# Performance work log

Hardware: AMD Instinct MI355X
Metric: run time of the kernel (lower is better)

The kernel has to match this reference:

```python
import jax, jax.numpy as jnp
import numpy as np

B, T, D = 8, 2048, 1024
H, C, DV = 8, 64, 128   # n_heads, latent_dim, d_head
LN_EPS = 1e-5
NORM_EPS = 1e-12  # F.normalize eps


def _xavier(k, shape, fan_in, fan_out):
    lim = float(np.sqrt(6.0 / (fan_in + fan_out)))
    return jax.random.uniform(k, shape, jnp.float32, -lim, lim)


def setup_inputs() -> dict:
    key = jax.random.key(0)
    ks = jax.random.split(key, 9)
    x = jax.random.normal(ks[0], (B, T, D), jnp.float32)
    Wq = _xavier(ks[1], (C, D), D, C)            # S_q weight (out,in)
    Wk = _xavier(ks[2], (C, D), D, C)            # S_k
    Wv = _xavier(ks[3], (C, D), D, C)            # S_v
    Qc = _xavier(ks[4], (H, C, C), C, C)         # per-head latent rotations
    Vc = _xavier(ks[5], (H, C, DV), C, DV)       # per-head value up-proj
    Wa_w = _xavier(ks[6], (H * C, D), D, H * C)  # W_alpha weight
    Wa_b = jnp.full((H * C,), 3.0, jnp.float32)  # W_alpha bias init = 3.0
    Wo = _xavier(ks[7], (D, H * DV), H * DV, D)  # output proj
    gamma = jnp.ones((D,), jnp.float32)
    beta = jnp.zeros((D,), jnp.float32)
    return {"x": x, "Wq": Wq, "Wk": Wk, "Wv": Wv, "Qc": Qc, "Vc": Vc,
            "Wa_w": Wa_w, "Wa_b": Wa_b, "Wo": Wo, "gamma": gamma, "beta": beta}


def _forward(x, Wq, Wk, Wv, Qc, Vc, Wa_w, Wa_b, Wo, gamma, beta):
    residual = x
    # LayerNorm (biased variance, like torch)
    mu = jnp.mean(x, axis=-1, keepdims=True)
    var = jnp.mean(jnp.square(x - mu), axis=-1, keepdims=True)
    xn = (x - mu) * jax.lax.rsqrt(var + LN_EPS) * gamma + beta

    q_lat = xn @ Wq.T          # (B,T,C)
    k_lat = xn @ Wk.T          # (B,T,C) shared across heads
    v_lat = xn @ Wv.T          # (B,T,C)

    q = jnp.einsum('btc,hce->bhte', q_lat, Qc)   # (B,H,T,C)
    v = jnp.einsum('btc,hcd->bhtd', v_lat, Vc)   # (B,H,T,DV)
    alpha = jax.nn.sigmoid(xn @ Wa_w.T + Wa_b)   # (B,T,H*C)
    alpha = alpha.reshape(x.shape[0], x.shape[1], H, C).transpose(0, 2, 1, 3)  # (B,H,T,C)

    # F.normalize(k, dim=-1): k / max(||k||, eps)
    kn = k_lat / jnp.maximum(jnp.linalg.norm(k_lat, axis=-1, keepdims=True), NORM_EPS)

    # time-major for scan
    qs = jnp.moveaxis(q, 2, 0)      # (T,B,H,C)
    vs = jnp.moveaxis(v, 2, 0)      # (T,B,H,DV)
    als = jnp.moveaxis(alpha, 2, 0)  # (T,B,H,C)
    kns = jnp.moveaxis(kn, 1, 0)    # (T,B,C)

    S0 = jnp.zeros((x.shape[0], H, C, DV), x.dtype)

    def step(S, inp):
        q_t, k_t, v_t, a_t = inp
        # S_t = diag(alpha_t) S_{t-1} + k_t v_t^T  (k shared across heads)
        S = a_t[..., None] * S + k_t[:, None, :, None] * v_t[..., None, :]
        o_t = jnp.einsum('bhcv,bhc->bhv', S, q_t)
        return S, o_t

    _, outs = jax.lax.scan(step, S0, (qs, kns, vs, als))  # outs: (T,B,H,DV)
    out = jnp.moveaxis(outs, 0, 1).reshape(x.shape[0], x.shape[1], H * DV)
    return out @ Wo.T + residual


def reference(x, Wq, Wk, Wv, Qc, Vc, Wa_w, Wa_b, Wo, gamma, beta):
    return _forward(x, Wq, Wk, Wv, Qc, Vc, Wa_w, Wa_b, Wo, gamma, beta)
```

## Files before the change

kernel.cpp:

```cpp
#include <hip/hip_runtime.h>

typedef unsigned short u16;
typedef unsigned int   u32;
typedef __bf16 bf16x8 __attribute__((ext_vector_type(8)));
typedef float  f32x4  __attribute__((ext_vector_type(4)));
typedef float  f32x8  __attribute__((ext_vector_type(8)));

#define B_  8
#define T_  2048
#define D_  1024
#define H_  8
#define C_  64
#define DV_ 128
#define M_  (B_*T_)
#define L_  128
#define NC_ (T_/L_)

__device__ __forceinline__ u16 f2bf(float f){
  u32 u = __float_as_uint(f);
  u32 r = (u + 0x7fffu + ((u >> 16) & 1u)) >> 16;
  return (u16)r;
}
__device__ __forceinline__ float bf2f(u16 u){
  return __uint_as_float(((u32)u) << 16);
}

typedef const __attribute__((address_space(1))) unsigned int* gp1_t;
typedef __attribute__((address_space(3))) unsigned int* lp3_t;
__device__ __forceinline__ void stage16(const void* g, void* l){
  __builtin_amdgcn_global_load_lds((gp1_t)g, (lp3_t)l, 16, 0, 0);
}

__global__ __launch_bounds__(256) void ln_kernel(
    const float* __restrict__ x, const float* __restrict__ gamma,
    const float* __restrict__ beta, u16* __restrict__ xnb){
  const int m = blockIdx.x;
  const int tid = threadIdx.x;
  const int wave = tid >> 6, lane = tid & 63;
  const float* xr = x + (size_t)m * D_;
  float4 xv = *(const float4*)&xr[tid*4];
  float s = xv.x + xv.y + xv.z + xv.w;
  #pragma unroll
  for (int off = 32; off > 0; off >>= 1) s += __shfl_xor(s, off, 64);
  __shared__ float red[8];
  if (lane == 0) red[wave] = s;
  __syncthreads();
  float mu = (red[0]+red[1]+red[2]+red[3]) * (1.f/1024.f);
  float dx = xv.x-mu, dy = xv.y-mu, dz = xv.z-mu, dw = xv.w-mu;
  float ss = dx*dx + dy*dy + dz*dz + dw*dw;
  #pragma unroll
  for (int off = 32; off > 0; off >>= 1) ss += __shfl_xor(ss, off, 64);
  if (lane == 0) red[4+wave] = ss;
  __syncthreads();
  float var = (red[4]+red[5]+red[6]+red[7]) * (1.f/1024.f);
  float rs = rsqrtf(var + 1e-5f);
  float4 g  = *(const float4*)&gamma[tid*4];
  float4 bb = *(const float4*)&beta[tid*4];
  ushort4 o4;
  o4.x = f2bf(dx*rs*g.x + bb.x);
  o4.y = f2bf(dy*rs*g.y + bb.y);
  o4.z = f2bf(dz*rs*g.z + bb.z);
  o4.w = f2bf(dw*rs*g.w + bb.w);
  *(ushort4*)&xnb[(size_t)m*D_ + tid*4] = o4;
}

__global__ __launch_bounds__(256) void prep_weights(
    const float* __restrict__ Wq, const float* __restrict__ Wk,
    const float* __restrict__ Wv, const float* __restrict__ Wa,
    const float* __restrict__ Qc, const float* __restrict__ Vc,
    const float* __restrict__ Wo,
    u16* __restrict__ Wcatb, u16* __restrict__ QcTb,
    u16* __restrict__ VcTb,  u16* __restrict__ Wob){
  int idx = blockIdx.x * 256 + threadIdx.x;
  if (idx < 786432){
    int r = idx >> 10, col = idx & 1023;
    float v = 0.f;
    if (r < 64)       v = Wq[(size_t)r*1024 + col];
    else if (r < 128) v = Wk[(size_t)(r-64)*1024 + col];
    else if (r < 192) v = Wv[(size_t)(r-128)*1024 + col];
    else if (r < 704) v = Wa[(size_t)(r-192)*1024 + col];
    Wcatb[idx] = f2bf(v);
  } else if (idx < 819200){
    int i = idx - 786432;
    int n = i >> 6, c = i & 63; int h = n >> 6, e = n & 63;
    QcTb[i] = f2bf(Qc[((size_t)h*64 + c)*64 + e]);
  } else if (idx < 884736){
    int i = idx - 819200;
    int n = i >> 6, c = i & 63; int h = n >> 7, d = n & 127;
    VcTb[i] = f2bf(Vc[((size_t)h*64 + c)*128 + d]);
  } else {
    int i = idx - 884736;
    Wob[i] = f2bf(Wo[i]);
  }
}

__global__ __launch_bounds__(256) void gemm_bf16(
    const u16* __restrict__ A, const u16* __restrict__ Bw,
    float* __restrict__ C, const float* __restrict__ res,
    u16* __restrict__ Cb, int N, int K){
  __shared__ __align__(16) u16 As[2][128*32];
  __shared__ __align__(16) u16 Bs[2][128*32];
  const int tid = threadIdx.x;
  const int wave = tid >> 6;
  const int lane = tid & 63;
  const int q  = lane >> 4;
  const int mr = lane & 15;
  const int wr = wave >> 1, wc = wave & 1;

  const int gx = gridDim.x;
  const int nlin = blockIdx.y * gx + blockIdx.x;
  const int chunk = (gx * gridDim.y) >> 3;
  const int swz = (nlin & 7) * chunk + (nlin >> 3);
  const int m0 = (swz % gx) * 128;
  const int n0 = (swz / gx) * 128;

  const int j0 = wave*2;
  const int lr = lane >> 2;
  const int slg = ((lane & 3) ^ ((lr >> 1) & 3)) * 8;
  const u16* pa0 = A  + (size_t)(m0 + (j0  )*16 + lr)*K + slg;
  const u16* pa1 = A  + (size_t)(m0 + (j0+1)*16 + lr)*K + slg;
  const u16* pb0 = Bw + (size_t)(n0 + (j0  )*16 + lr)*K + slg;
  const u16* pb1 = Bw + (size_t)(n0 + (j0+1)*16 + lr)*K + slg;
  u16* la0 = &As[0][(j0  )*512];
  u16* la1 = &As[0][(j0+1)*512];
  u16* lb0 = &Bs[0][(j0  )*512];
  u16* lb1 = &Bs[0][(j0+1)*512];
  const int bufstride = 128*32;

  union FragU { uint4 u4; bf16x8 v; };
  f32x4 zero = {0.f, 0.f, 0.f, 0.f};
  f32x4 acc[4][4];
  #pragma unroll
  for (int i = 0; i < 4; i++)
    #pragma unroll
    for (int j = 0; j < 4; j++) acc[i][j] = zero;

  const int qs = (q ^ ((mr >> 1) & 3)) * 8;
  const int aoff = (wr*64 + mr)*32 + qs;
  const int boff = (wc*64 + mr)*32 + qs;

  stage16(pa0, la0); stage16(pa1, la1);
  stage16(pb0, lb0); stage16(pb1, lb1);
  __syncthreads();

  int p = 0;
  for (int k0 = 0; k0 < K; k0 += 32){
    if (k0 + 32 < K){
      int pn = p ^ 1;
      stage16(pa0 + k0 + 32, la0 + pn*bufstride);
      stage16(pa1 + k0 + 32, la1 + pn*bufstride);
      stage16(pb0 + k0 + 32, lb0 + pn*bufstride);
      stage16(pb1 + k0 + 32, lb1 + pn*bufstride);
    }
    bf16x8 afr[4], bfr[4];
    #pragma unroll
    for (int mt = 0; mt < 4; mt++){
      FragU f; f.u4 = *(const uint4*)(&As[p][aoff + mt*512]);
      afr[mt] = f.v;
    }
    #pragma unroll
    for (int nt = 0; nt < 4; nt++){
      FragU f; f.u4 = *(const uint4*)(&Bs[p][boff + nt*512]);
      bfr[nt] = f.v;
    }
    #pragma unroll
    for (int mt = 0; mt < 4; mt++)
      #pragma unroll
      for (int nt = 0; nt < 4; nt++)
        acc[mt][nt] = __builtin_amdgcn_mfma_f32_16x16x32_bf16(
            afr[mt], bfr[nt], acc[mt][nt], 0, 0, 0);
    __syncthreads();
    p ^= 1;
  }

  #pragma unroll
  for (int mt = 0; mt < 4; mt++)
    #pragma unroll
    for (int nt = 0; nt < 4; nt++){
      int col = n0 + wc*64 + nt*16 + mr;
      if (col < N){
        #pragma unroll
        for (int r = 0; r < 4; r++){
          int row = m0 + wr*64 + mt*16 + q*4 + r;
          size_t idx = (size_t)row * N + col;
          float v = acc[mt][nt][r];
          if (res) v += res[idx];
          if (Cb) Cb[idx] = f2bf(v);
          else    C[idx] = v;
        }
      }
    }
}

__global__ __launch_bounds__(256) void split_proj(
    const float* __restrict__ proj, const float* __restrict__ Wab,
    u16* __restrict__ qlatb, float* __restrict__ knf,
    u16* __restrict__ vlatb, float* __restrict__ alphaf){
  const int m = blockIdx.x * 4 + (threadIdx.x >> 6);
  const int lane = threadIdx.x & 63;
  const float* pr = proj + (size_t)m * 704;
  qlatb[(size_t)m*64 + lane] = f2bf(pr[lane]);
  float kv = pr[64 + lane];
  float ss = kv * kv;
  #pragma unroll
  for (int off = 32; off > 0; off >>= 1) ss += __shfl_xor(ss, off, 64);
  float nrm = fmaxf(sqrtf(ss), 1e-12f);
  knf[(size_t)m*64 + lane] = kv / nrm;
  vlatb[(size_t)m*64 + lane] = f2bf(pr[128 + lane]);
  #pragma unroll
  for (int j = 0; j < 8; j++){
    int jj = j*64 + lane;
    float av = pr[192 + jj] + Wab[jj];
    alphaf[(size_t)m*512 + jj] = 1.f / (1.f + expf(-av));
  }
}


__global__ __launch_bounds__(512, 8) void scan_pass1(
    const float* __restrict__ knf, const u16* __restrict__ vb,
    const float* __restrict__ alphaf,
    float* __restrict__ Sbuf, float* __restrict__ btot){
  const int ch = blockIdx.x;
  const int bh = blockIdx.y;
  const int b = bh >> 3, h = bh & 7;
  const int tid = threadIdx.x;
  const int w = __builtin_amdgcn_readfirstlane(tid >> 6);
  const int dg = tid & 63;
  const int t0 = ch * L_;

  const float* kp  = knf    + ((size_t)(b*T_ + t0))*64  + w*8;
  const float* ap  = alphaf + ((size_t)(b*T_ + t0))*512 + h*64 + w*8;
  const float* alp = ap + (dg & 7);
  const u32*   vp  = (const u32*)(vb + ((size_t)(b*T_ + t0))*1024 + h*128) + dg;

  float S[8][2];
  #pragma unroll
  for (int j = 0; j < 8; j++){ S[j][0] = 0.f; S[j][1] = 0.f; }
  float bt = 1.f;

  for (int t = 0; t < L_; t += 2){
    f32x8 a0, a1, k0, k1;
    asm volatile(
      "s_load_dwordx8 %0, %4, 0x0\n\t"
      "s_load_dwordx8 %1, %4, 0x800\n\t"
      "s_load_dwordx8 %2, %5, 0x0\n\t"
      "s_load_dwordx8 %3, %5, 0x100\n\t"
      "s_waitcnt lgkmcnt(0)"
      : "=&s"(a0), "=&s"(a1), "=&s"(k0), "=&s"(k1)
      : "s"(ap), "s"(kp));
    float al0 = alp[0], al1 = alp[512];
    u32 vv0 = vp[0], vv1 = vp[512];
    float v00 = __uint_as_float(vv0 << 16);
    float v01 = __uint_as_float(vv0 & 0xffff0000u);
    float v10 = __uint_as_float(vv1 << 16);
    float v11 = __uint_as_float(vv1 & 0xffff0000u);
    #pragma unroll
    for (int j = 0; j < 8; j++){
      S[j][0] = a0[j]*S[j][0] + k0[j]*v00;
      S[j][1] = a0[j]*S[j][1] + k0[j]*v01;
    }
    bt *= al0;
    #pragma unroll
    for (int j = 0; j < 8; j++){
      S[j][0] = a1[j]*S[j][0] + k1[j]*v10;
      S[j][1] = a1[j]*S[j][1] + k1[j]*v11;
    }
    bt *= al1;
    ap += 1024; kp += 128; alp += 1024; vp += 1024;
  }

  float* Sl = Sbuf + ((size_t)bh*NC_ + ch) * (64*128);
  #pragma unroll
  for (int j = 0; j < 8; j++)
    *(float2*)&Sl[(size_t)(w*8+j)*128 + 2*dg] = make_float2(S[j][0], S[j][1]);
  if (dg < 8) btot[((size_t)bh*NC_ + ch)*64 + w*8 + dg] = bt;
}

__global__ __launch_bounds__(256) void scan_combine(
    float* __restrict__ Sbuf, const float* __restrict__ btot){
  const int bh = blockIdx.y;
  const int e  = blockIdx.x * 256 + threadIdx.x;
  float*       Sb  = Sbuf + (size_t)bh*NC_*8192 + e;
  const float* btb = btot + (size_t)bh*NC_*64 + (e >> 7);
  float S = 0.f;
  #pragma unroll
  for (int j = 0; j < NC_; j++){
    float loc = Sb[(size_t)j*8192];
    Sb[(size_t)j*8192] = S;
    if (j < NC_-1) S = btb[j*64] * S + loc;
  }
}

__global__ __launch_bounds__(512, 8) void scan_pass2(
    const float* __restrict__ qf, const float* __restrict__ knf,
    const u16* __restrict__ vb, const float* __restrict__ alphaf,
    const float* __restrict__ Sbuf, u16* __restrict__ ob){
  const int ch = blockIdx.x;
  const int bh = blockIdx.y;
  const int b = bh >> 3, h = bh & 7;
  const int tid = threadIdx.x;
  const int w = __builtin_amdgcn_readfirstlane(tid >> 6);
  const int dg = tid & 63;
  const int t0 = ch * L_;
  __shared__ __align__(16) float sO[2][8][4][128];

  const float* qp = qf     + ((size_t)(b*T_ + t0))*512 + h*64 + w*8;
  const float* kp = knf    + ((size_t)(b*T_ + t0))*64  + w*8;
  const float* ap = alphaf + ((size_t)(b*T_ + t0))*512 + h*64 + w*8;
  const u32*   vp = (const u32*)(vb + ((size_t)(b*T_ + t0))*1024 + h*128) + dg;
  u16* obase = ob + ((size_t)(b*T_ + t0))*1024 + h*128;

  float S[8][2];
  const float* Si = Sbuf + ((size_t)bh*NC_ + ch) * (64*128);
  #pragma unroll
  for (int j = 0; j < 8; j++){
    float2 s2 = *(const float2*)&Si[(size_t)(w*8+j)*128 + 2*dg];
    S[j][0] = s2.x; S[j][1] = s2.y;
  }

  const int rtt = tid >> 7, rdd = tid & 127;

  for (int sb = 0; sb < L_/4; sb++){
    const int p = sb & 1;
    #pragma unroll
    for (int half = 0; half < 2; half++){
      f32x8 a0, a1, k0, k1, q0, q1;
      asm volatile(
        "s_load_dwordx8 %0, %6, 0x0\n\t"
        "s_load_dwordx8 %1, %6, 0x800\n\t"
        "s_load_dwordx8 %2, %7, 0x0\n\t"
        "s_load_dwordx8 %3, %7, 0x100\n\t"
        "s_load_dwordx8 %4, %8, 0x0\n\t"
        "s_load_dwordx8 %5, %8, 0x800\n\t"
        "s_waitcnt lgkmcnt(0)"
        : "=&s"(a0), "=&s"(a1), "=&s"(k0), "=&s"(k1), "=&s"(q0), "=&s"(q1)
        : "s"(ap), "s"(kp), "s"(qp));
      u32 vv0 = vp[0], vv1 = vp[512];
      float v00 = __uint_as_float(vv0 << 16);
      float v01 = __uint_as_float(vv0 & 0xffff0000u);
      float v10 = __uint_as_float(vv1 << 16);
      float v11 = __uint_as_float(vv1 & 0xffff0000u);
      {
        float oa0, oa1, ob0, ob1;
        S[0][0] = a0[0]*S[0][0] + k0[0]*v00;  oa0 = S[0][0]*q0[0];
        S[0][1] = a0[0]*S[0][1] + k0[0]*v01;  oa1 = S[0][1]*q0[0];
        S[1][0] = a0[1]*S[1][0] + k0[1]*v00;  ob0 = S[1][0]*q0[1];
        S[1][1] = a0[1]*S[1][1] + k0[1]*v01;  ob1 = S[1][1]*q0[1];
        #pragma unroll
        for (int j = 2; j < 8; j += 2){
          S[j][0]   = a0[j]*S[j][0]     + k0[j]*v00;    oa0 += S[j][0]*q0[j];
          S[j][1]   = a0[j]*S[j][1]     + k0[j]*v01;    oa1 += S[j][1]*q0[j];
          S[j+1][0] = a0[j+1]*S[j+1][0] + k0[j+1]*v00;  ob0 += S[j+1][0]*q0[j+1];
          S[j+1][1] = a0[j+1]*S[j+1][1] + k0[j+1]*v01;  ob1 += S[j+1][1]*q0[j+1];
        }
        *(float2*)&sO[p][w][half*2+0][2*dg] = make_float2(oa0+ob0, oa1+ob1);
      }
      {
        float oa0, oa1, ob0, ob1;
        S[0][0] = a1[0]*S[0][0] + k1[0]*v10;  oa0 = S[0][0]*q1[0];
        S[0][1] = a1[0]*S[0][1] + k1[0]*v11;  oa1 = S[0][1]*q1[0];
        S[1][0] = a1[1]*S[1][0] + k1[1]*v10;  ob0 = S[1][0]*q1[1];
        S[1][1] = a1[1]*S[1][1] + k1[1]*v11;  ob1 = S[1][1]*q1[1];
        #pragma unroll
        for (int j = 2; j < 8; j += 2){
          S[j][0]   = a1[j]*S[j][0]     + k1[j]*v10;    oa0 += S[j][0]*q1[j];
          S[j][1]   = a1[j]*S[j][1]     + k1[j]*v11;    oa1 += S[j][1]*q1[j];
          S[j+1][0] = a1[j+1]*S[j+1][0] + k1[j+1]*v10;  ob0 += S[j+1][0]*q1[j+1];
          S[j+1][1] = a1[j+1]*S[j+1][1] + k1[j+1]*v11;  ob1 += S[j+1][1]*q1[j+1];
        }
        *(float2*)&sO[p][w][half*2+1][2*dg] = make_float2(oa0+ob0, oa1+ob1);
      }
      ap += 1024; kp += 128; qp += 1024; vp += 1024;
    }
    __syncthreads();
    float o = sO[p][0][rtt][rdd] + sO[p][1][rtt][rdd]
            + sO[p][2][rtt][rdd] + sO[p][3][rtt][rdd]
            + sO[p][4][rtt][rdd] + sO[p][5][rtt][rdd]
            + sO[p][6][rtt][rdd] + sO[p][7][rtt][rdd];
    obase[(size_t)(sb*4 + rtt)*1024 + rdd] = f2bf(o);
  }
}

extern "C" void kernel_launch(void* const* d_in, const int* in_sizes, int n_in,
                              void* d_out, int out_size, void* d_ws, size_t ws_size,
                              hipStream_t stream){
  const float* x     = (const float*)d_in[0];
  const float* Wq    = (const float*)d_in[1];
  const float* Wk    = (const float*)d_in[2];
  const float* Wv    = (const float*)d_in[3];
  const float* Qc    = (const float*)d_in[4];
  const float* Vc    = (const float*)d_in[5];
  const float* Wa_w  = (const float*)d_in[6];
  const float* Wa_b  = (const float*)d_in[7];
  const float* Wo    = (const float*)d_in[8];
  const float* gamma = (const float*)d_in[9];
  const float* beta  = (const float*)d_in[10];
  float* out = (float*)d_out;

  char* ws = (char*)d_ws;
  size_t off = 0;
  auto alloc = [&](size_t bytes) -> void* {
    void* p = ws + off; off += (bytes + 255) & ~(size_t)255; return p;
  };
  char* R1 = (char*)alloc((size_t)M_ * 1024 * 2);
  u16*   xnb  = (u16*)R1;
  u16*   obuf = (u16*)R1;
  char* R2 = (char*)alloc((size_t)M_ * 704 * 4);
  float* proj = (float*)R2;
  float* qf   = (float*)R2;
  float* Sbuf   = (float*)alloc((size_t)64 * NC_ * 8192 * 4);
  u16*   vfb    = (u16*)alloc((size_t)M_ * 1024 * 2);
  float* alphaf = (float*)alloc((size_t)M_ * 512 * 4);
  float* knf    = (float*)alloc((size_t)M_ * 64 * 4);
  u16*   qlatb  = (u16*)alloc((size_t)M_ * 64 * 2);
  u16*   vlatb  = (u16*)alloc((size_t)M_ * 64 * 2);
  u16*   Wcatb  = (u16*)alloc((size_t)768 * 1024 * 2);
  u16*   QcTb   = (u16*)alloc((size_t)512 * 64 * 2);
  u16*   VcTb   = (u16*)alloc((size_t)1024 * 64 * 2);
  u16*   Wob    = (u16*)alloc((size_t)1024 * 1024 * 2);
  float* btotp  = (float*)alloc((size_t)64 * NC_ * 64 * 4);
  (void)ws_size; (void)in_sizes; (void)n_in; (void)out_size;

  ln_kernel<<<dim3(M_), dim3(256), 0, stream>>>(x, gamma, beta, xnb);
  prep_weights<<<dim3(7552), dim3(256), 0, stream>>>(
      Wq, Wk, Wv, Wa_w, Qc, Vc, Wo, Wcatb, QcTb, VcTb, Wob);
  gemm_bf16<<<dim3(M_/128, 6), dim3(256), 0, stream>>>(
      xnb, Wcatb, proj, nullptr, nullptr, 704, 1024);
  split_proj<<<dim3(M_/4), dim3(256), 0, stream>>>(
      proj, Wa_b, qlatb, knf, vlatb, alphaf);
  gemm_bf16<<<dim3(M_/128, 8), dim3(256), 0, stream>>>(
      vlatb, VcTb, nullptr, nullptr, vfb, 1024, 64);
  gemm_bf16<<<dim3(M_/128, 4), dim3(256), 0, stream>>>(
      qlatb, QcTb, qf, nullptr, nullptr, 512, 64);
  scan_pass1<<<dim3(NC_-1, 64), dim3(512), 0, stream>>>(
      knf, vfb, alphaf, Sbuf, btotp);
  scan_combine<<<dim3(32, 64), dim3(256), 0, stream>>>(Sbuf, btotp);
  scan_pass2<<<dim3(NC_, 64), dim3(512), 0, stream>>>(
      qf, knf, vfb, alphaf, Sbuf, obuf);
  gemm_bf16<<<dim3(M_/128, 8), dim3(256), 0, stream>>>(
      obuf, Wob, out, x, nullptr, 1024, 1024);
}
```

Baseline: 513.1 us.

## Triple-buffer GEMM LDS staging with explicit vmcnt waits and drop tile swizzle

The bf16 GEMM moves from double to triple buffering of the A/B LDS tiles, with loads issued two tiles ahead. Waits are now partial s_waitcnt vmcnt plus raw s_barrier instead of full __syncthreads, so more global-to-LDS traffic overlaps MFMA work. It also removes the grouped block-index swizzle in favour of plain blockIdx mapping. That may reduce L2 reuse across blocks, and the extra buffer raises LDS use per block, which could lower occupancy.

New measurement: 510.0 us. No clear change (-0.6%).

```diff
diff --git a/kernel.cpp b/kernel.cpp
--- a/kernel.cpp
+++ b/kernel.cpp
@@ -30,6 +30,13 @@
 __device__ __forceinline__ void stage16(const void* g, void* l){
   __builtin_amdgcn_global_load_lds((gp1_t)g, (lp3_t)l, 16, 0, 0);
 }
+
+#define VMCNT(N) asm volatile("s_waitcnt vmcnt(" #N ")" ::: "memory")
+#define SBAR() do{ asm volatile("" ::: "memory"); \
+                   __builtin_amdgcn_sched_barrier(0); \
+                   __builtin_amdgcn_s_barrier(); \
+                   __builtin_amdgcn_sched_barrier(0); \
+                   asm volatile("" ::: "memory"); }while(0)
 
 __global__ __launch_bounds__(256) void ln_kernel(
     const float* __restrict__ x, const float* __restrict__ gamma,
@@ -98,21 +105,16 @@
     const u16* __restrict__ A, const u16* __restrict__ Bw,
     float* __restrict__ C, const float* __restrict__ res,
     u16* __restrict__ Cb, int N, int K){
-  __shared__ __align__(16) u16 As[2][128*32];
-  __shared__ __align__(16) u16 Bs[2][128*32];
+  __shared__ __align__(16) u16 As[3][128*32];
+  __shared__ __align__(16) u16 Bs[3][128*32];
   const int tid = threadIdx.x;
   const int wave = tid >> 6;
   const int lane = tid & 63;
   const int q  = lane >> 4;
   const int mr = lane & 15;
   const int wr = wave >> 1, wc = wave & 1;
-
-  const int gx = gridDim.x;
-  const int nlin = blockIdx.y * gx + blockIdx.x;
-  const int chunk = (gx * gridDim.y) >> 3;
-  const int swz = (nlin & 7) * chunk + (nlin >> 3);
-  const int m0 = (swz % gx) * 128;
-  const int n0 = (swz / gx) * 128;
+  const int m0 = blockIdx.x * 128;
+  const int n0 = blockIdx.y * 128;
 
   const int j0 = wave*2;
   const int lr = lane >> 2;
@@ -121,11 +123,6 @@
   const u16* pa1 = A  + (size_t)(m0 + (j0+1)*16 + lr)*K + slg;
   const u16* pb0 = Bw + (size_t)(n0 + (j0  )*16 + lr)*K + slg;
   const u16* pb1 = Bw + (size_t)(n0 + (j0+1)*16 + lr)*K + slg;
-  u16* la0 = &As[0][(j0  )*512];
-  u16* la1 = &As[0][(j0+1)*512];
-  u16* lb0 = &Bs[0][(j0  )*512];
-  u16* lb1 = &Bs[0][(j0+1)*512];
-  const int bufstride = 128*32;
 
   union FragU { uint4 u4; bf16x8 v; };
   f32x4 zero = {0.f, 0.f, 0.f, 0.f};
@@ -139,51 +136,70 @@
   const int aoff = (wr*64 + mr)*32 + qs;
   const int boff = (wc*64 + mr)*32 + qs;
 
-  stage16(pa0, la0); stage16(pa1, la1);
-  stage16(pb0, lb0); stage16(pb1, lb1);
-  __syncthreads();
-
-  int p = 0;
-  for (int k0 = 0; k0 < K; k0 += 32){
-    if (k0 + 32 < K){
-      int pn = p ^ 1;
-      stage16(pa0 + k0 + 32, la0 + pn*bufstride);
-      stage16(pa1 + k0 + 32, la1 + pn*bufstride);
-      stage16(pb0 + k0 + 32, lb0 + pn*bufstride);
-      stage16(pb1 + k0 + 32, lb1 + pn*bufstride);
-    }
+  auto stage_tile = [&](int t, int b){
+    int off = t*32;
+    stage16(pa0 + off, &As[b][(j0  )*512]);
+    stage16(pa1 + off, &As[b][(j0+1)*512]);
+    stage16(pb0 + off, &Bs[b][(j0  )*512]);
+    stage16(pb1 + off, &Bs[b][(j0+1)*512]);
+  };
+  auto compute = [&](int b){
     bf16x8 afr[4], bfr[4];
     #pragma unroll
     for (int mt = 0; mt < 4; mt++){
-      FragU f; f.u4 = *(const uint4*)(&As[p][aoff + mt*512]);
+      FragU f; f.u4 = *(const uint4*)(&As[b][aoff + mt*512]);
       afr[mt] = f.v;
     }
     #pragma unroll
-    for (int nt = 0; nt < 4; nt++){
-      FragU f; f.u4 = *(const uint4*)(&Bs[p][boff + nt*512]);
-      bfr[nt] = f.v;
+    for (int nt2 = 0; nt2 < 4; nt2++){
+      FragU f; f.u4 = *(const uint4*)(&Bs[b][boff + nt2*512]);
+      bfr[nt2] = f.v;
     }
     #pragma unroll
     for (int mt = 0; mt < 4; mt++)
       #pragma unroll
-      for (int nt = 0; nt < 4; nt++)
-        acc[mt][nt] = __builtin_amdgcn_mfma_f32_16x16x32_bf16(
-            afr[mt], bfr[nt], acc[mt][nt], 0, 0, 0);
-    __syncthreads();
-    p ^= 1;
-  }
+      for (int nt2 = 0; nt2 < 4; nt2++)
+        acc[mt][nt2] = __builtin_amdgcn_mfma_f32_16x16x32_bf16(
+            afr[mt], bfr[nt2], acc[mt][nt2], 0, 0, 0);
+  };
+
+  const int nt = K >> 5;
+  stage_tile(0, 0);
+  if (nt > 1) stage_tile(1, 1);
+
+  int bcur = 0;
+  int bst  = 2;
+  for (int i = 0; i < nt-2; i++){
+    stage_tile(i+2, bst);
+    VMCNT(8);
+    SBAR();
+    compute(bcur);
+    SBAR();
+    bcur = (bcur == 2) ? 0 : bcur + 1;
+    bst  = (bst  == 2) ? 0 : bst  + 1;
+  }
+  if (nt >= 2){
+    VMCNT(4);
+    SBAR();
+    compute(bcur);
+    SBAR();
+    bcur = (bcur == 2) ? 0 : bcur + 1;
+  }
+  VMCNT(0);
+  SBAR();
+  compute(bcur);
 
   #pragma unroll
   for (int mt = 0; mt < 4; mt++)
     #pragma unroll
-    for (int nt = 0; nt < 4; nt++){
-      int col = n0 + wc*64 + nt*16 + mr;
+    for (int nt2 = 0; nt2 < 4; nt2++){
+      int col = n0 + wc*64 + nt2*16 + mr;
       if (col < N){
         #pragma unroll
         for (int r = 0; r < 4; r++){
           int row = m0 + wr*64 + mt*16 + q*4 + r;
           size_t idx = (size_t)row * N + col;
-          float v = acc[mt][nt][r];
+          float v = acc[mt][nt2][r];
           if (res) v += res[idx];
           if (Cb) Cb[idx] = f2bf(v);
           else    C[idx] = v;
```
